# Kernel optimization log

Hardware: AMD Instinct MI355X
Metric: run time of the kernel (lower is better)

Reference implementation:

```python
import jax, jax.numpy as jnp
import numpy as np

EMBED_DIM = 1024
NUM_HEADS = 16
HEAD_DIM = EMBED_DIM // NUM_HEADS
LN_EPS = 1e-5


def setup_inputs() -> dict:
    key = jax.random.key(0)
    ks = jax.random.split(key, 13)
    b, n_q, k_len, E = 4, 2048, 2048, EMBED_DIM
    s = 1.0 / np.sqrt(E)
    inp = {
        "Q_input": jax.random.normal(ks[0], (b, n_q, E), jnp.float32),
        "K_input": jax.random.normal(ks[1], (b, k_len, E), jnp.float32),
        "V_input": jax.random.normal(ks[2], (b, k_len, E), jnp.float32),
        "Wq": jax.random.normal(ks[3], (E, E), jnp.float32) * s,
        "bq": jnp.zeros((E,), jnp.float32),
        "Wk": jax.random.normal(ks[4], (E, E), jnp.float32) * s,
        "bk": jnp.zeros((E,), jnp.float32),
        "Wv": jax.random.normal(ks[5], (E, E), jnp.float32) * s,
        "bv": jnp.zeros((E,), jnp.float32),
        "Wo": jax.random.normal(ks[6], (E, E), jnp.float32) * s,
        "bo": jnp.zeros((E,), jnp.float32),
        "gamma": jnp.ones((E,), jnp.float32),
        "beta": jnp.zeros((E,), jnp.float32),
    }
    return inp


def _layer_norm(x, gamma, beta):
    mu = jnp.mean(x, axis=-1, keepdims=True)
    var = jnp.mean(jnp.square(x - mu), axis=-1, keepdims=True)
    return (x - mu) * jax.lax.rsqrt(var + LN_EPS) * gamma + beta


def reference(Q_input, K_input, V_input, Wq, bq, Wk, bk, Wv, bv, Wo, bo, gamma, beta):
    b, n_q, E = Q_input.shape
    k_len = K_input.shape[1]
    H, D = NUM_HEADS, HEAD_DIM
    # projections (Linear: x @ W^T + b; here W stored as [E_in, E_out])
    Q = (Q_input @ Wq + bq).reshape(b, n_q, H, D).transpose(0, 2, 1, 3)   # [b,H,n_q,D]
    K = (K_input @ Wk + bk).reshape(b, k_len, H, D).transpose(0, 2, 1, 3)  # [b,H,k,D]
    V = (V_input @ Wv + bv).reshape(b, k_len, H, D).transpose(0, 2, 1, 3)
    scores = jnp.einsum('bhqd,bhkd->bhqk', Q, K) / jnp.sqrt(jnp.float32(D))
    attn = jax.nn.softmax(scores, axis=-1)
    ctx = jnp.einsum('bhqk,bhkd->bhqd', attn, V)           # [b,H,n_q,D]
    ctx = ctx.transpose(0, 2, 1, 3).reshape(b, n_q, E)
    out = ctx @ Wo + bo                                    # dropout = identity (eval)
    return _layer_norm(Q_input + out, gamma, beta)
```

## Files before the change

### kernel.cpp

```cpp
#include <hip/hip_runtime.h>

typedef __attribute__((ext_vector_type(8))) short s8v;
typedef __attribute__((ext_vector_type(4))) short s4v;
typedef __attribute__((ext_vector_type(4))) float f4v;

#define MFMA16(a, b, c) __builtin_amdgcn_mfma_f32_16x16x32_bf16((a), (b), (c), 0, 0, 0)
#define AS1 __attribute__((address_space(1)))
#define AS3 __attribute__((address_space(3)))

__device__ __forceinline__ short f2bf(float f) {
  union { float f; unsigned u; } v; v.f = f;
  unsigned r = v.u + 0x7FFFu + ((v.u >> 16) & 1u);
  return (short)(r >> 16);
}
__device__ __forceinline__ unsigned fbits(float f) {
  union { float f; unsigned u; } v; v.f = f; return v.u;
}
__device__ __forceinline__ unsigned pack2(float hi, float lo) {
  return __builtin_amdgcn_perm(fbits(hi), fbits(lo), 0x07060302u);
}
__device__ __forceinline__ void gld16(const void* g, void* l) {
  __builtin_amdgcn_global_load_lds((const AS1 unsigned*)g, (AS3 unsigned*)l, 16, 0, 0);
}

__global__ __launch_bounds__(256) void castbf(const float* __restrict__ in,
                                              short* __restrict__ out) {
  int g = blockIdx.x * 256 + threadIdx.x;
  for (int i = 0; i < 4; ++i) {
    int idx = g + i * 524288;
    float4 v = ((const float4*)in)[idx];
    s4v o = { f2bf(v.x), f2bf(v.y), f2bf(v.z), f2bf(v.w) };
    ((s4v*)out)[idx] = o;
  }
}

__global__ __launch_bounds__(256) void wtrans(const float* __restrict__ W,
                                              short* __restrict__ Wt) {
  __shared__ float tile[64][65];
  const int r0 = blockIdx.y * 64, c0 = blockIdx.x * 64;
  const int t = threadIdx.x;
  for (int i = 0; i < 4; ++i) {
    int lin = t + i * 256;
    int row = lin >> 4, c4 = (lin & 15) << 2;
    float4 v = *(const float4*)(W + (size_t)(r0 + row) * 1024 + c0 + c4);
    tile[row][c4 + 0] = v.x; tile[row][c4 + 1] = v.y;
    tile[row][c4 + 2] = v.z; tile[row][c4 + 3] = v.w;
  }
  __syncthreads();
  for (int i = 0; i < 4; ++i) {
    int lin = t + i * 256;
    int nl = lin >> 4, k4 = (lin & 15) << 2;
    s4v sv = { f2bf(tile[k4 + 0][nl]), f2bf(tile[k4 + 1][nl]),
               f2bf(tile[k4 + 2][nl]), f2bf(tile[k4 + 3][nl]) };
    *(s4v*)&Wt[(size_t)(c0 + nl) * 1024 + r0 + k4] = sv;
  }
}

template <int OUT>
__global__ __launch_bounds__(256) void gemm_bt(
    const short* __restrict__ A, const short* __restrict__ Bt,
    const float* __restrict__ bias, float scale,
    short* __restrict__ outb, float* __restrict__ outf) {
  __shared__ __align__(16) short As[128 * 32];
  __shared__ __align__(16) short Bs[128 * 32];
  const int tid = threadIdx.x;
  const int lane = tid & 63, w = tid >> 6;
  const int quad = lane >> 4, l16 = lane & 15;
  const int wm = (w >> 1) * 64, wn = (w & 1) * 64;
  const int mBase = blockIdx.y * 128, nBase = blockIdx.x * 128;
  f4v acc[4][4] = {};

  const int id0 = tid, id1 = tid + 256;
  const int r0 = id0 >> 2, c0 = (id0 & 3) << 3;
  const int r1 = id1 >> 2, c1 = (id1 & 3) << 3;
  const short* Ag0 = A + (size_t)(mBase + r0) * 1024 + c0;
  const short* Ag1 = A + (size_t)(mBase + r1) * 1024 + c1;
  const short* Bg0 = Bt + (size_t)(nBase + r0) * 1024 + c0;
  const short* Bg1 = Bt + (size_t)(nBase + r1) * 1024 + c1;

  for (int kt = 0; kt < 32; ++kt) {
    __syncthreads();
    gld16(Ag0 + kt * 32, &As[id0 * 8]);
    gld16(Ag1 + kt * 32, &As[id1 * 8]);
    gld16(Bg0 + kt * 32, &Bs[id0 * 8]);
    gld16(Bg1 + kt * 32, &Bs[id1 * 8]);
    __syncthreads();
    s8v a[4], b[4];
    for (int mt = 0; mt < 4; ++mt) a[mt] = *(const s8v*)&As[(wm + mt * 16 + l16) * 32 + quad * 8];
    for (int nt = 0; nt < 4; ++nt) b[nt] = *(const s8v*)&Bs[(wn + nt * 16 + l16) * 32 + quad * 8];
    for (int mt = 0; mt < 4; ++mt)
      for (int nt = 0; nt < 4; ++nt)
        acc[mt][nt] = MFMA16(a[mt], b[nt], acc[mt][nt]);
  }

  for (int nt = 0; nt < 4; ++nt) {
    int col = nBase + wn + nt * 16 + l16;
    float bs = bias[col];
    for (int mt = 0; mt < 4; ++mt) {
      for (int r = 0; r < 4; ++r) {
        int row = mBase + wm + mt * 16 + quad * 4 + r;
        float val = (acc[mt][nt][r] + bs) * scale;
        if constexpr (OUT == 0) {
          int b = row >> 11, token = row & 2047, h = col >> 6, d = col & 63;
          outb[(((size_t)b * 16 + h) * 2048 + token) * 64 + d] = f2bf(val);
        } else if constexpr (OUT == 2) {
          int b = row >> 11, token = row & 2047, h = col >> 6, d = col & 63;
          outb[(((size_t)b * 16 + h) * 64 + d) * 2048 + token] = f2bf(val);
        } else {
          outf[(size_t)row * 1024 + col] = val;
        }
      }
    }
  }
}

__global__ __launch_bounds__(256, 2) void attn_kernel(
    const short* __restrict__ Qp, const short* __restrict__ Kp,
    const short* __restrict__ Vpt, short* __restrict__ Ctx) {
  __shared__ __align__(16) short Ks[64][72];
  __shared__ __align__(16) short Vt[64][72];

  const int tid = threadIdx.x, w = tid >> 6, lane = tid & 63;
  const int quad = lane >> 4, l16 = lane & 15;
  const int qt = blockIdx.x, bh = blockIdx.y;
  const short* Qb = Qp + (size_t)bh * 2048 * 64;
  const short* Kb = Kp + (size_t)bh * 2048 * 64;
  const short* Vb = Vpt + (size_t)bh * 64 * 2048;
  const int qbase = qt * 256 + w * 64;

  s8v qf[4][2];
#pragma unroll
  for (int mt = 0; mt < 4; ++mt)
#pragma unroll
    for (int h = 0; h < 2; ++h)
      qf[mt][h] = *(const s8v*)(Qb + (size_t)(qbase + mt * 16 + l16) * 64 + h * 32 + quad * 8);

  const s8v vone = {16256, 16256, 16256, 16256, 16256, 16256, 16256, 16256};
  f4v Oa[4][4] = {};
  f4v La[4] = {};

  for (int kv = 0; kv < 32; ++kv) {
    const int kv0 = kv * 64;
    __syncthreads();
#pragma unroll
    for (int i = 0; i < 2; ++i) {
      int id = tid + i * 256;
      int g = id >> 3, c8 = (id & 7) << 3;
      int p = (g & 32) | (((g >> 2) & 1) << 4) | (((g >> 3) & 3) << 2) | (g & 3);
      *(s8v*)&Ks[p][c8] = *(const s8v*)(Kb + (size_t)(kv0 + g) * 64 + c8);
      *(s8v*)&Vt[g][c8] = *(const s8v*)(Vb + (size_t)g * 2048 + kv0 + c8);
    }
    __syncthreads();

    s8v kf[4][2], vf[4][2];
#pragma unroll
    for (int T = 0; T < 4; ++T) {
      kf[T][0] = *(const s8v*)&Ks[T * 16 + l16][quad * 8];
      kf[T][1] = *(const s8v*)&Ks[T * 16 + l16][32 + quad * 8];
      vf[T][0] = *(const s8v*)&Vt[T * 16 + l16][quad * 8];
      vf[T][1] = *(const s8v*)&Vt[T * 16 + l16][32 + quad * 8];
    }

#pragma unroll
    for (int mt = 0; mt < 4; ++mt) {
      f4v s[4] = {};
#pragma unroll
      for (int T = 0; T < 4; ++T) {
        s[T] = MFMA16(kf[T][0], qf[mt][0], s[T]);
        s[T] = MFMA16(kf[T][1], qf[mt][1], s[T]);
      }
#pragma unroll
      for (int T = 0; T < 4; ++T)
#pragma unroll
        for (int r = 0; r < 4; ++r)
          s[T][r] = __builtin_amdgcn_exp2f(s[T][r]);
      s8v pf[2];
#pragma unroll
      for (int cp = 0; cp < 2; ++cp) {
        union { s8v v; unsigned u[4]; } pk;
        pk.u[0] = pack2(s[2 * cp][1], s[2 * cp][0]);
        pk.u[1] = pack2(s[2 * cp][3], s[2 * cp][2]);
        pk.u[2] = pack2(s[2 * cp + 1][1], s[2 * cp + 1][0]);
        pk.u[3] = pack2(s[2 * cp + 1][3], s[2 * cp + 1][2]);
        pf[cp] = pk.v;
      }
      La[mt] = MFMA16(pf[0], vone, La[mt]);
      La[mt] = MFMA16(pf[1], vone, La[mt]);
#pragma unroll
      for (int nt = 0; nt < 4; ++nt) {
        Oa[mt][nt] = MFMA16(pf[0], vf[nt][0], Oa[mt][nt]);
        Oa[mt][nt] = MFMA16(pf[1], vf[nt][1], Oa[mt][nt]);
      }
    }
  }

  const int b = bh >> 4, h = bh & 15;
#pragma unroll
  for (int mt = 0; mt < 4; ++mt)
#pragma unroll
    for (int r = 0; r < 4; ++r) {
      float inv = 1.f / La[mt][r];
      int q = qbase + mt * 16 + quad * 4 + r;
#pragma unroll
      for (int nt = 0; nt < 4; ++nt) {
        int d = nt * 16 + l16;
        Ctx[((size_t)b * 2048 + q) * 1024 + h * 64 + d] = f2bf(Oa[mt][nt][r] * inv);
      }
    }
}

__global__ __launch_bounds__(256) void ln_kernel(
    const float* __restrict__ resid, const float* __restrict__ attn,
    const float* __restrict__ gamma, const float* __restrict__ beta,
    float* __restrict__ out) {
  const int row = blockIdx.x, t = threadIdx.x;
  const float4 rv = *(const float4*)(resid + (size_t)row * 1024 + t * 4);
  const float4 av = *(const float4*)(attn + (size_t)row * 1024 + t * 4);
  float x0 = rv.x + av.x, x1 = rv.y + av.y, x2 = rv.z + av.z, x3 = rv.w + av.w;
  float s = x0 + x1 + x2 + x3;
  float ss = x0 * x0 + x1 * x1 + x2 * x2 + x3 * x3;
  for (int off = 32; off > 0; off >>= 1) {
    s += __shfl_down(s, off, 64);
    ss += __shfl_down(ss, off, 64);
  }
  __shared__ float red[8];
  const int wid = t >> 6, lane = t & 63;
  if (lane == 0) { red[wid] = s; red[4 + wid] = ss; }
  __syncthreads();
  float S = red[0] + red[1] + red[2] + red[3];
  float SS = red[4] + red[5] + red[6] + red[7];
  float mu = S * (1.f / 1024.f);
  float var = SS * (1.f / 1024.f) - mu * mu;
  float rstd = rsqrtf(var + 1e-5f);
  const float4 g = *(const float4*)(gamma + t * 4);
  const float4 bb = *(const float4*)(beta + t * 4);
  float4 o;
  o.x = (x0 - mu) * rstd * g.x + bb.x;
  o.y = (x1 - mu) * rstd * g.y + bb.y;
  o.z = (x2 - mu) * rstd * g.z + bb.z;
  o.w = (x3 - mu) * rstd * g.w + bb.w;
  *(float4*)(out + (size_t)row * 1024 + t * 4) = o;
}

extern "C" void kernel_launch(void* const* d_in, const int* in_sizes, int n_in,
                              void* d_out, int out_size, void* d_ws, size_t ws_size,
                              hipStream_t stream) {
  const float* Qin = (const float*)d_in[0];
  const float* Kin = (const float*)d_in[1];
  const float* Vin = (const float*)d_in[2];
  const float* Wq = (const float*)d_in[3];
  const float* bq = (const float*)d_in[4];
  const float* Wk = (const float*)d_in[5];
  const float* bk = (const float*)d_in[6];
  const float* Wv = (const float*)d_in[7];
  const float* bv = (const float*)d_in[8];
  const float* Wo = (const float*)d_in[9];
  const float* bo = (const float*)d_in[10];
  const float* gamma = (const float*)d_in[11];
  const float* beta = (const float*)d_in[12];
  float* out = (float*)d_out;

  char* ws = (char*)d_ws;
  const size_t MB = 1024 * 1024;
  short* Ab  = (short*)(ws);
  short* Qp  = (short*)(ws + 16 * MB);
  short* Kp  = (short*)(ws + 32 * MB);
  short* Vpt = (short*)(ws + 48 * MB);
  short* Ctx = (short*)(ws + 64 * MB);
  short* Wqt = (short*)(ws + 80 * MB);
  short* Wkt = (short*)(ws + 82 * MB);
  short* Wvt = (short*)(ws + 84 * MB);
  short* Wot = (short*)(ws + 86 * MB);
  float* AOut = (float*)(ws);

  dim3 tg(16, 16);
  wtrans<<<tg, 256, 0, stream>>>(Wq, Wqt);
  wtrans<<<tg, 256, 0, stream>>>(Wk, Wkt);
  wtrans<<<tg, 256, 0, stream>>>(Wv, Wvt);
  wtrans<<<tg, 256, 0, stream>>>(Wo, Wot);

  const float qscale = 0.125f * 1.44269504f;
  dim3 gg(8, 64);
  castbf<<<2048, 256, 0, stream>>>(Qin, Ab);
  gemm_bt<0><<<gg, 256, 0, stream>>>(Ab, Wqt, bq, qscale, Qp, nullptr);
  castbf<<<2048, 256, 0, stream>>>(Kin, Ab);
  gemm_bt<0><<<gg, 256, 0, stream>>>(Ab, Wkt, bk, 1.f, Kp, nullptr);
  castbf<<<2048, 256, 0, stream>>>(Vin, Ab);
  gemm_bt<2><<<gg, 256, 0, stream>>>(Ab, Wvt, bv, 1.f, Vpt, nullptr);

  attn_kernel<<<dim3(8, 64), 256, 0, stream>>>(Qp, Kp, Vpt, Ctx);

  gemm_bt<1><<<gg, 256, 0, stream>>>(Ctx, Wot, bo, 1.f, nullptr, AOut);

  ln_kernel<<<8192, 256, 0, stream>>>(Qin, AOut, gamma, beta, out);
}
```

Measured before the change: 381.4 us.

## Batch weight transposes and Q/K projections into single launches, stage V transpose through LDS

Merges the four weight-transpose launches into one 3D grid, and casts plus projects Q and K together with a z-dimension batch, cutting launch count and filling more CUs per launch. The V projection epilogue now stages its transposed tile in shared memory and writes 16-byte vectors along the token dimension instead of scattered 2-byte stores. The grid mapping is swapped so blockIdx.x walks M. The workspace layout is reshuffled so Q and K sit contiguously, at the cost of an extra LDS buffer in the V epilogue.

Result: faster. 363.7 us (-4.7%).

```diff
diff --git a/kernel.cpp b/kernel.cpp
--- a/kernel.cpp
+++ b/kernel.cpp
@@ -23,8 +23,11 @@
   __builtin_amdgcn_global_load_lds((const AS1 unsigned*)g, (AS3 unsigned*)l, 16, 0, 0);
 }
 
-__global__ __launch_bounds__(256) void castbf(const float* __restrict__ in,
+__global__ __launch_bounds__(256) void castbf(const float* __restrict__ in0,
+                                              const float* __restrict__ in1,
                                               short* __restrict__ out) {
+  const float* in = blockIdx.y ? in1 : in0;
+  out += (size_t)blockIdx.y * 8388608;
   int g = blockIdx.x * 256 + threadIdx.x;
   for (int i = 0; i < 4; ++i) {
     int idx = g + i * 524288;
@@ -34,8 +37,13 @@
   }
 }
 
-__global__ __launch_bounds__(256) void wtrans(const float* __restrict__ W,
-                                              short* __restrict__ Wt) {
+__global__ __launch_bounds__(256) void wtrans4(const float* __restrict__ W0,
+                                               const float* __restrict__ W1,
+                                               const float* __restrict__ W2,
+                                               const float* __restrict__ W3,
+                                               short* __restrict__ Wt) {
+  const float* W = blockIdx.z == 0 ? W0 : blockIdx.z == 1 ? W1 : blockIdx.z == 2 ? W2 : W3;
+  Wt += (size_t)blockIdx.z * 1048576;
   __shared__ float tile[64][65];
   const int r0 = blockIdx.y * 64, c0 = blockIdx.x * 64;
   const int t = threadIdx.x;
@@ -59,15 +67,23 @@
 template <int OUT>
 __global__ __launch_bounds__(256) void gemm_bt(
     const short* __restrict__ A, const short* __restrict__ Bt,
-    const float* __restrict__ bias, float scale,
+    const float* __restrict__ bias0, const float* __restrict__ bias1,
+    float s0, float s1,
     short* __restrict__ outb, float* __restrict__ outf) {
   __shared__ __align__(16) short As[128 * 32];
   __shared__ __align__(16) short Bs[128 * 32];
+  const int z = blockIdx.z;
+  A += (size_t)z * 8388608;
+  Bt += (size_t)z * 1048576;
+  outb += (size_t)z * 8388608;
+  const float* bias = z ? bias1 : bias0;
+  const float scale = z ? s1 : s0;
+
   const int tid = threadIdx.x;
   const int lane = tid & 63, w = tid >> 6;
   const int quad = lane >> 4, l16 = lane & 15;
   const int wm = (w >> 1) * 64, wn = (w & 1) * 64;
-  const int mBase = blockIdx.y * 128, nBase = blockIdx.x * 128;
+  const int mBase = blockIdx.x * 128, nBase = blockIdx.y * 128;
   f4v acc[4][4] = {};
 
   const int id0 = tid, id1 = tid + 256;
@@ -93,21 +109,40 @@
         acc[mt][nt] = MFMA16(a[mt], b[nt], acc[mt][nt]);
   }
 
-  for (int nt = 0; nt < 4; ++nt) {
-    int col = nBase + wn + nt * 16 + l16;
-    float bs = bias[col];
-    for (int mt = 0; mt < 4; ++mt) {
-      for (int r = 0; r < 4; ++r) {
-        int row = mBase + wm + mt * 16 + quad * 4 + r;
-        float val = (acc[mt][nt][r] + bs) * scale;
-        if constexpr (OUT == 0) {
-          int b = row >> 11, token = row & 2047, h = col >> 6, d = col & 63;
-          outb[(((size_t)b * 16 + h) * 2048 + token) * 64 + d] = f2bf(val);
-        } else if constexpr (OUT == 2) {
-          int b = row >> 11, token = row & 2047, h = col >> 6, d = col & 63;
-          outb[(((size_t)b * 16 + h) * 64 + d) * 2048 + token] = f2bf(val);
-        } else {
-          outf[(size_t)row * 1024 + col] = val;
+  if constexpr (OUT == 2) {
+    __shared__ short Ts[128 * 136];
+    for (int nt = 0; nt < 4; ++nt) {
+      int colg = nBase + wn + nt * 16 + l16;
+      float bs = bias[colg];
+      for (int mt = 0; mt < 4; ++mt)
+        for (int r = 0; r < 4; ++r)
+          Ts[(wn + nt * 16 + l16) * 136 + wm + mt * 16 + quad * 4 + r] =
+              f2bf(acc[mt][nt][r] + bs);
+    }
+    __syncthreads();
+    const int bI = mBase >> 11, tok0 = mBase & 2047;
+    for (int it = 0; it < 8; ++it) {
+      int dloc = (tid >> 4) + it * 16;
+      int tok8 = (tid & 15) << 3;
+      s8v v = *(const s8v*)&Ts[dloc * 136 + tok8];
+      int colg = nBase + dloc;
+      int h = colg >> 6, d = colg & 63;
+      *(s8v*)&outb[(((size_t)bI * 16 + h) * 64 + d) * 2048 + tok0 + tok8] = v;
+    }
+  } else {
+    for (int nt = 0; nt < 4; ++nt) {
+      int col = nBase + wn + nt * 16 + l16;
+      float bs = bias[col];
+      for (int mt = 0; mt < 4; ++mt) {
+        for (int r = 0; r < 4; ++r) {
+          int row = mBase + wm + mt * 16 + quad * 4 + r;
+          float val = (acc[mt][nt][r] + bs) * scale;
+          if constexpr (OUT == 0) {
+            int b = row >> 11, token = row & 2047, h = col >> 6, d = col & 63;
+            outb[(((size_t)b * 16 + h) * 2048 + token) * 64 + d] = f2bf(val);
+          } else {
+            outf[(size_t)row * 1024 + col] = val;
+          }
         }
       }
     }
@@ -263,34 +298,26 @@
   char* ws = (char*)d_ws;
   const size_t MB = 1024 * 1024;
   short* Ab  = (short*)(ws);
-  short* Qp  = (short*)(ws + 16 * MB);
-  short* Kp  = (short*)(ws + 32 * MB);
-  short* Vpt = (short*)(ws + 48 * MB);
-  short* Ctx = (short*)(ws + 64 * MB);
-  short* Wqt = (short*)(ws + 80 * MB);
-  short* Wkt = (short*)(ws + 82 * MB);
-  short* Wvt = (short*)(ws + 84 * MB);
-  short* Wot = (short*)(ws + 86 * MB);
-  float* AOut = (float*)(ws);
-
-  dim3 tg(16, 16);
-  wtrans<<<tg, 256, 0, stream>>>(Wq, Wqt);
-  wtrans<<<tg, 256, 0, stream>>>(Wk, Wkt);
-  wtrans<<<tg, 256, 0, stream>>>(Wv, Wvt);
-  wtrans<<<tg, 256, 0, stream>>>(Wo, Wot);
+  short* Qp  = (short*)(ws + 32 * MB);
+  short* Kp  = (short*)(ws + 48 * MB);
+  short* Vpt = (short*)(ws + 64 * MB);
+  short* Wt  = (short*)(ws + 80 * MB);
+  short* Ctx = (short*)(ws);
+  float* AOut = (float*)(ws + 16 * MB);
+
+  wtrans4<<<dim3(16, 16, 4), 256, 0, stream>>>(Wq, Wk, Wv, Wo, Wt);
 
   const float qscale = 0.125f * 1.44269504f;
-  dim3 gg(8, 64);
-  castbf<<<2048, 256, 0, stream>>>(Qin, Ab);
-  gemm_bt<0><<<gg, 256, 0, stream>>>(Ab, Wqt, bq, qscale, Qp, nullptr);
-  castbf<<<2048, 256, 0, stream>>>(Kin, Ab);
-  gemm_bt<0><<<gg, 256, 0, stream>>>(Ab, Wkt, bk, 1.f, Kp, nullptr);
-  castbf<<<2048, 256, 0, stream>>>(Vin, Ab);
-  gemm_bt<2><<<gg, 256, 0, stream>>>(Ab, Wvt, bv, 1.f, Vpt, nullptr);
+
+  castbf<<<dim3(2048, 2), 256, 0, stream>>>(Qin, Kin, Ab);
+  gemm_bt<0><<<dim3(64, 8, 2), 256, 0, stream>>>(Ab, Wt, bq, bk, qscale, 1.f, Qp, nullptr);
+
+  castbf<<<dim3(2048, 1), 256, 0, stream>>>(Vin, nullptr, Ab);
+  gemm_bt<2><<<dim3(64, 8, 1), 256, 0, stream>>>(Ab, Wt + 2 * 1048576, bv, nullptr, 1.f, 0.f, Vpt, nullptr);
 
   attn_kernel<<<dim3(8, 64), 256, 0, stream>>>(Qp, Kp, Vpt, Ctx);
 
-  gemm_bt<1><<<gg, 256, 0, stream>>>(Ctx, Wot, bo, 1.f, nullptr, AOut);
+  gemm_bt<1><<<dim3(64, 8, 1), 256, 0, stream>>>(Ctx, Wt + 3 * 1048576, bo, nullptr, 1.f, 0.f, nullptr, AOut);
 
   ln_kernel<<<8192, 256, 0, stream>>>(Qin, AOut, gamma, beta, out);
 }
```
